# Performance work log

Measured on AMD Instinct MI355X. Metric: run time of the kernel, lower is better.

Reference implementation:

```python
import jax, jax.numpy as jnp
import numpy as np

N = 2_000_000
D = 128
S = 100_000


def setup_inputs() -> dict:
    key = jax.random.key(0)
    k1, k2, k3 = jax.random.split(key, 3)
    # small scale keeps exp(logit) well within fp32 range
    features = jax.random.normal(k1, (N, D), dtype=jnp.float32) * 0.05
    w = jax.random.normal(k2, (D,), dtype=jnp.float32) * 0.05
    phrase_id = jax.random.randint(k3, (N,), 0, S)
    unique_phrase = jnp.arange(S)
    return {"features": features, "w": w, "phrase_id": phrase_id,
            "unique_phrase": unique_phrase}


def reference(features, w, phrase_id, unique_phrase):
    # logit_i = exp(gamma(features)_i), gamma is a bias-free Linear(D, 1)
    logit = jnp.exp(features @ w)                               # [N]
    # per-segment partition function via scatter-add, then gather back
    partition = jax.ops.segment_sum(logit, phrase_id,
                                    num_segments=unique_phrase.shape[0])  # [S]
    weights = logit / partition[phrase_id]                      # [N]
    return weights[:, None]                                     # [N, 1]
```

## Files before the change

kernel.cpp:

```cpp
#include <hip/hip_runtime.h>


__global__ void logit_partition_kernel(const float4* __restrict__ F4,
                                       const float* __restrict__ w,
                                       const int* __restrict__ pid,
                                       float* __restrict__ logit,
                                       float* __restrict__ part,
                                       int nrows) {
    const int lane = threadIdx.x & 63;
    const int l32  = lane & 31;
    const int half = lane >> 5;
    const int wave  = (blockIdx.x * blockDim.x + threadIdx.x) >> 6;
    const int nwave = (gridDim.x * blockDim.x) >> 6;

    const float4 wf = reinterpret_cast<const float4*>(w)[l32];

    for (int r = wave * 2; r < nrows; r += nwave * 2) {
        const int row = r + half;
        if (row < nrows) {
            float4 f = F4[(size_t)row * 32 + l32];
            float s = f.x * wf.x + f.y * wf.y + f.z * wf.z + f.w * wf.w;
            #pragma unroll
            for (int o = 16; o; o >>= 1) s += __shfl_xor(s, o, 64);
            if (l32 == 0) {
                float lg = expf(s);
                logit[row] = lg;
                atomicAdd(&part[pid[row]], lg);
            }
        }
    }
}

__global__ void weights_kernel(const float4* __restrict__ logit4,
                               const int4* __restrict__ pid4,
                               const float* __restrict__ part,
                               float4* __restrict__ out4,
                               int nvec,
                               const float* __restrict__ logit,
                               const int* __restrict__ pid,
                               float* __restrict__ out,
                               int n) {
    int i = blockIdx.x * blockDim.x + threadIdx.x;
    const int stride = gridDim.x * blockDim.x;
    for (; i < nvec; i += stride) {
        float4 lg = logit4[i];
        int4 p = pid4[i];
        float4 o;
        o.x = lg.x / part[p.x];
        o.y = lg.y / part[p.y];
        o.z = lg.z / part[p.z];
        o.w = lg.w / part[p.w];
        out4[i] = o;
    }
    if (blockIdx.x == 0 && threadIdx.x == 0) {
        for (int j = nvec * 4; j < n; ++j) out[j] = logit[j] / part[pid[j]];
    }
}

extern "C" void kernel_launch(void* const* d_in, const int* in_sizes, int n_in,
                              void* d_out, int out_size, void* d_ws, size_t ws_size,
                              hipStream_t stream) {
    const float* features = (const float*)d_in[0];
    const float* w        = (const float*)d_in[1];
    const int*   pid      = (const int*)d_in[2];

    const int N = in_sizes[2];
    const int S = in_sizes[3];

    float* logit = (float*)d_ws;
    float* part  = logit + N;
    float* out   = (float*)d_out;

    hipMemsetAsync(part, 0, (size_t)S * sizeof(float), stream);

    {
        dim3 grid(2048), block(256);
        logit_partition_kernel<<<grid, block, 0, stream>>>(
            (const float4*)features, w, pid, logit, part, N);
    }

    {
        const int nvec = N / 4;
        int blocks = (nvec + 255) / 256;
        if (blocks > 2048) blocks = 2048;
        weights_kernel<<<dim3(blocks), dim3(256), 0, stream>>>(
            (const float4*)logit, (const int4*)pid, part, (float4*)out, nvec,
            logit, pid, out, N);
    }
}
```

Measured before the change: 256.1 us.

## Batch 16 rows per wave with transposed shuffle reduction in logit kernel

Each wave now loads 8 float4 feature chunks (16 rows) up front before reducing, which raises memory-level parallelism. The per-row butterfly reductions are merged into a single transpose-style reduction, so more lanes finish holding useful sums and fewer shuffles are needed. Four lanes per half then issue exp, store and atomicAdd in parallel instead of one lane per row. This adds register pressure and more complex index logic, with a scalar tail loop kept for leftover rows.

```diff
diff --git a/kernel.cpp b/kernel.cpp
--- a/kernel.cpp
+++ b/kernel.cpp
@@ -15,7 +15,53 @@
 
     const float4 wf = reinterpret_cast<const float4*>(w)[l32];
 
-    for (int r = wave * 2; r < nrows; r += nwave * 2) {
+    const int ntile = nrows / 16;
+    const int nmain = ntile * 16;
+
+    for (int t = wave; t < ntile; t += nwave) {
+        const int r = t * 16;
+
+        float4 f[8];
+        #pragma unroll
+        for (int j = 0; j < 8; ++j)
+            f[j] = F4[(size_t)(r + 2 * j + half) * 32 + l32];
+
+        float s[8];
+        #pragma unroll
+        for (int j = 0; j < 8; ++j)
+            s[j] = f[j].x * wf.x + f[j].y * wf.y + f[j].z * wf.z + f[j].w * wf.w;
+
+        float m[4];
+        #pragma unroll
+        for (int j = 0; j < 4; ++j) {
+            float u = s[2*j]   + __shfl_xor(s[2*j],   16, 64);
+            float v = s[2*j+1] + __shfl_xor(s[2*j+1], 16, 64);
+            m[j] = (l32 & 16) ? v : u;
+        }
+        float n[2];
+        #pragma unroll
+        for (int j = 0; j < 2; ++j) {
+            float u = m[2*j]   + __shfl_xor(m[2*j],   8, 64);
+            float v = m[2*j+1] + __shfl_xor(m[2*j+1], 8, 64);
+            n[j] = (l32 & 8) ? v : u;
+        }
+        float u = n[0] + __shfl_xor(n[0], 4, 64);
+        float v = n[1] + __shfl_xor(n[1], 4, 64);
+        float tt = (l32 & 4) ? v : u;
+        tt += __shfl_xor(tt, 2, 64);
+        tt += __shfl_xor(tt, 1, 64);
+
+        if ((l32 & 3) == 0) {
+            const int jidx = ((l32 >> 2) & 1) * 4 + ((l32 >> 3) & 1) * 2 +
+                             ((l32 >> 4) & 1);
+            const int row = r + 2 * jidx + half;
+            float lg = expf(tt);
+            logit[row] = lg;
+            atomicAdd(&part[pid[row]], lg);
+        }
+    }
+
+    for (int r = nmain + wave * 2; r < nrows; r += nwave * 2) {
         const int row = r + half;
         if (row < nrows) {
             float4 f = F4[(size_t)row * 32 + l32];
@@ -73,11 +119,8 @@
 
     hipMemsetAsync(part, 0, (size_t)S * sizeof(float), stream);
 
-    {
-        dim3 grid(2048), block(256);
-        logit_partition_kernel<<<grid, block, 0, stream>>>(
-            (const float4*)features, w, pid, logit, part, N);
-    }
+    logit_partition_kernel<<<dim3(2048), dim3(256), 0, stream>>>(
+        (const float4*)features, w, pid, logit, part, N);
 
     {
         const int nvec = N / 4;
```

After: 229.8 us. 1.11x faster.
